# Performance work log

Measured on AMD Instinct MI355X. Metric: run time of the kernel, lower is better.

## Reference

```python
import jax, jax.numpy as jnp
import numpy as np

T, H, E, I, K = 2048, 2048, 16, 512, 2
ROUTED_SCALE = 1.5   # config.moe_router_scaling_factor
SWIGLU_LIMIT = 7.0   # config.swiglu_limits[layer_id]


def setup_inputs() -> dict:
    key = jax.random.key(0)
    k1, k2, k3, k4, k5 = jax.random.split(key, 5)
    hidden_states = jax.random.normal(k1, (T, H), jnp.float32)
    gate_w = jax.random.normal(k2, (E, H), jnp.float32) * 0.02
    router_bias = jax.random.normal(k3, (E,), jnp.float32) * 0.01
    w13 = jax.random.normal(k4, (E, 2 * I, H), jnp.float32) * 0.02  # [gate; up] fused
    w2 = jax.random.normal(k5, (E, H, I), jnp.float32) * 0.02
    return {"hidden_states": hidden_states, "gate_w": gate_w,
            "router_bias": router_bias, "w13": w13, "w2": w2, "top_k": K}


def reference(hidden_states, gate_w, router_bias, w13, w2, top_k):
    n_tok = hidden_states.shape[0]
    n_exp = gate_w.shape[0]
    # fp32 gate (need_fp32_gate=True)
    router_logits = hidden_states.astype(jnp.float32) @ gate_w.T          # [T, E]
    scores = jax.nn.sigmoid(router_logits)
    # correction bias only affects expert choice, not the combine weights
    _, topk_ids = jax.lax.top_k(scores + router_bias[None, :], top_k)     # [T, K]
    topk_w = jnp.take_along_axis(scores, topk_ids, axis=1)                # [T, K]
    topk_w = topk_w / jnp.sum(topk_w, axis=1, keepdims=True)              # renormalize
    topk_w = topk_w * ROUTED_SCALE
    # scatter routing weights into dense per-expert combine weights [T, E]
    comb = jnp.zeros((n_tok, n_exp), jnp.float32)
    comb = comb.at[jnp.arange(n_tok)[:, None], topk_ids].add(topk_w)
    # expert SwiGLU MLPs, dense over experts (zero combine weight == not routed)
    gu = jnp.einsum('th,eoh->teo', hidden_states, w13)                    # [T, E, 2I]
    g, u = jnp.split(gu, 2, axis=-1)
    g = jnp.minimum(g, SWIGLU_LIMIT)                                      # gemm1_clamp_limit
    u = jnp.clip(u, -SWIGLU_LIMIT, SWIGLU_LIMIT)
    act = g * jax.nn.sigmoid(g) * u                                       # silu(gate) * up
    expert_out = jnp.einsum('tei,ehi->teh', act, w2)                      # [T, E, H]
    return jnp.einsum('teh,te->th', expert_out, comb)                     # [T, H]
```

## Files before the change

### kernel.cpp

```cpp
#include <hip/hip_runtime.h>
#include <hip/hip_bf16.h>
#include <math.h>

#define T_TOK 2048
#define H_DIM 2048
#define E_EXP 16
#define I_DIM 512
#define TWO_I 1024
#define ROUTED_SCALE 1.5f
#define SWIGLU_LIMIT 7.0f

#define BM 64
#define KC 64
#define MAX_TILES 80

typedef __attribute__((ext_vector_type(8))) short bf16x8;
typedef __attribute__((ext_vector_type(4))) float f32x4;
typedef unsigned short u16;

__device__ inline u16 f2bf(float f) {
    return __builtin_bit_cast(u16, __float2bfloat16(f));
}
__device__ inline ushort4 pack4(float4 a) {
    ushort4 v;
    v.x = f2bf(a.x); v.y = f2bf(a.y); v.z = f2bf(a.z); v.w = f2bf(a.w);
    return v;
}

__device__ inline void gload16(const u16* g, u16* l) {
    __builtin_amdgcn_global_load_lds(
        (const __attribute__((address_space(1))) void*)(g),
        (__attribute__((address_space(3))) void*)(l), 16, 0, 0);
}

#define SWZ(row, k) ((row) * 64 + ((k) ^ (((row) & 7) << 3)))

__global__ __launch_bounds__(256) void router_kernel(
    const float* __restrict__ hs, const float* __restrict__ gw,
    const float* __restrict__ bias, int* cnt, int* tok_list, float* w_list,
    u16* __restrict__ hs_bf)
{
    int wave = threadIdx.x >> 6;
    int lane = threadIdx.x & 63;
    int t = blockIdx.x * 4 + wave;
    if (t >= T_TOK) return;
    const float* x = hs + (size_t)t * H_DIM;

    float acc[E_EXP];
#pragma unroll
    for (int e = 0; e < E_EXP; ++e) acc[e] = 0.f;

#pragma unroll 2
    for (int c = 0; c < 8; ++c) {
        int col = c * 256 + lane * 4;
        float4 xv = *(const float4*)(x + col);
        *(ushort4*)(hs_bf + (size_t)t * H_DIM + col) = pack4(xv);
#pragma unroll
        for (int e = 0; e < E_EXP; ++e) {
            float4 gv = *(const float4*)(gw + (size_t)e * H_DIM + col);
            acc[e] = fmaf(xv.x, gv.x, acc[e]);
            acc[e] = fmaf(xv.y, gv.y, acc[e]);
            acc[e] = fmaf(xv.z, gv.z, acc[e]);
            acc[e] = fmaf(xv.w, gv.w, acc[e]);
        }
    }
#pragma unroll
    for (int e = 0; e < E_EXP; ++e) {
        for (int m = 32; m >= 1; m >>= 1)
            acc[e] += __shfl_xor(acc[e], m, 64);
    }
    if (lane == 0) {
        float sc[E_EXP], bsc[E_EXP];
#pragma unroll
        for (int e = 0; e < E_EXP; ++e) {
            sc[e] = 1.f / (1.f + expf(-acc[e]));
            bsc[e] = sc[e] + bias[e];
        }
        int e0 = 0; float b0 = bsc[0];
#pragma unroll
        for (int e = 1; e < E_EXP; ++e) if (bsc[e] > b0) { b0 = bsc[e]; e0 = e; }
        int e1 = -1; float b1 = -1e30f;
#pragma unroll
        for (int e = 0; e < E_EXP; ++e) {
            if (e == e0) continue;
            if (bsc[e] > b1) { b1 = bsc[e]; e1 = e; }
        }
        float s0 = sc[e0], s1 = sc[e1];
        float inv = ROUTED_SCALE / (s0 + s1);
        int p0 = atomicAdd(&cnt[e0], 1);
        tok_list[e0 * T_TOK + p0] = t;
        w_list[e0 * T_TOK + p0] = s0 * inv;
        int p1 = atomicAdd(&cnt[e1], 1);
        tok_list[e1 * T_TOK + p1] = t;
        w_list[e1 * T_TOK + p1] = s1 * inv;
    }
}

__global__ void scatter_build(const int* __restrict__ cnt,
    const int* __restrict__ tok_list, const float* __restrict__ w_list,
    int* A_tok, float* A_w, int* tile_e, int* tile_r0)
{
    int c[E_EXP], offs[E_EXP + 1];
    offs[0] = 0;
#pragma unroll
    for (int e = 0; e < E_EXP; ++e) {
        c[e] = cnt[e];
        offs[e + 1] = offs[e] + ((c[e] + BM - 1) & ~(BM - 1));
    }
    int idx = blockIdx.x * 256 + threadIdx.x;
    int e = idx >> 11;
    int pos = idx & (T_TOK - 1);
    int ce = c[e];
    int pe = (ce + BM - 1) & ~(BM - 1);
    if (pos < ce) {
        A_tok[offs[e] + pos] = tok_list[idx];
        A_w[offs[e] + pos] = w_list[idx];
    } else if (pos < pe) {
        A_tok[offs[e] + pos] = -1;
        A_w[offs[e] + pos] = 0.f;
    }
    if (idx == 0) {
        int nt = 0;
        for (int ee = 0; ee < E_EXP; ++ee) {
            int ntile = (c[ee] + BM - 1) >> 6;
            for (int j = 0; j < ntile; ++j) {
                tile_e[nt] = ee;
                tile_r0[nt] = offs[ee] + j * BM;
                ++nt;
            }
        }
        for (; nt < MAX_TILES; ++nt) tile_e[nt] = -1;
    }
}

__global__ __launch_bounds__(256, 3) void gemm1_act(
    const u16* __restrict__ hs_bf, const float* __restrict__ w13,
    const int* __restrict__ A_tok, const int* __restrict__ tile_e,
    const int* __restrict__ tile_r0, u16* __restrict__ act)
{
    int b = blockIdx.x;
    int id = (b & 7) * 80 + (b >> 3);
    int tile = id % MAX_TILES;
    int y = id / MAX_TILES;
    int e = tile_e[tile];
    if (e < 0) return;
    int row0 = tile_r0[tile];
    int i0 = y * 64;
    int tid = threadIdx.x;

    __shared__ u16 Xs[2][4096];
    __shared__ u16 Gs[2][4096];
    __shared__ u16 Us[2][4096];

    const int l = tid & 63, w = tid >> 6;

    const int rlo = l >> 3;
    const int c8 = (l & 7) << 3;
    const int ksrc = c8 ^ (rlo << 3);
    const int rowA = w * 16 + rlo;
    const int rowB = rowA + 8;
    int tokA = A_tok[row0 + rowA]; if (tokA < 0) tokA = 0;
    int tokB = A_tok[row0 + rowB]; if (tokB < 0) tokB = 0;
    const u16* sXA = hs_bf + (size_t)tokA * H_DIM + ksrc;
    const u16* sXB = hs_bf + (size_t)tokB * H_DIM + ksrc;
    const int dA = w * 1024;

#define X_STAGE(bb, t) do { int ko = (t) * KC; \
    gload16(sXA + ko, &Xs[bb][dA]);  gload16(sXB + ko, &Xs[bb][dA + 512]); } while (0)

    const int srow = tid >> 4;
    const int sc4  = tid & 15;
    const int kphys = (sc4 * 4) ^ ((srow & 7) << 3);
    const int sbase = srow * 64 + kphys;
    const float* gsrc = w13 + ((size_t)e * TWO_I + i0 + srow) * H_DIM + sc4 * 4;
    const float* usrc = gsrc + (size_t)I_DIM * H_DIM;

    float4 gld[4], uld[4];
#define W_LOAD(t) do { int k0 = (t) * KC; \
    gld[0] = *(const float4*)(gsrc + k0); \
    gld[1] = *(const float4*)(gsrc + k0 + 16 * H_DIM); \
    gld[2] = *(const float4*)(gsrc + k0 + 32 * H_DIM); \
    gld[3] = *(const float4*)(gsrc + k0 + 48 * H_DIM); \
    uld[0] = *(const float4*)(usrc + k0); \
    uld[1] = *(const float4*)(usrc + k0 + 16 * H_DIM); \
    uld[2] = *(const float4*)(usrc + k0 + 32 * H_DIM); \
    uld[3] = *(const float4*)(usrc + k0 + 48 * H_DIM); } while (0)

#define W_WRITE(bb) do { \
    *(ushort4*)&Gs[bb][sbase]        = pack4(gld[0]); \
    *(ushort4*)&Gs[bb][sbase + 1024] = pack4(gld[1]); \
    *(ushort4*)&Gs[bb][sbase + 2048] = pack4(gld[2]); \
    *(ushort4*)&Gs[bb][sbase + 3072] = pack4(gld[3]); \
    *(ushort4*)&Us[bb][sbase]        = pack4(uld[0]); \
    *(ushort4*)&Us[bb][sbase + 1024] = pack4(uld[1]); \
    *(ushort4*)&Us[bb][sbase + 2048] = pack4(uld[2]); \
    *(ushort4*)&Us[bb][sbase + 3072] = pack4(uld[3]); } while (0)

    const int wm = w >> 1, wn = w & 1;
    const int lr = l & 15;
    const int lg = l >> 4;
    const int ra0 = wm * 32 + lr, ra1 = ra0 + 16;
    const int rb0 = wn * 32 + lr, rb1 = rb0 + 16;
    int ia0[2], ia1[2], ib0[2], ib1[2];
#pragma unroll
    for (int kh = 0; kh < 2; ++kh) {
        int e2 = kh * 32 + lg * 8;
        ia0[kh] = SWZ(ra0, e2); ia1[kh] = SWZ(ra1, e2);
        ib0[kh] = SWZ(rb0, e2); ib1[kh] = SWZ(rb1, e2);
    }

    const f32x4 Z4 = {0.f, 0.f, 0.f, 0.f};
    f32x4 aG[2][2], aU[2][2];
#pragma unroll
    for (int m = 0; m < 2; ++m)
#pragma unroll
        for (int n = 0; n < 2; ++n) { aG[m][n] = Z4; aU[m][n] = Z4; }

    W_LOAD(0);
    X_STAGE(0, 0);
    W_WRITE(0);
    __syncthreads();
    int cur = 0;
    const int NT = H_DIM / KC;
    for (int t = 0; t < NT; ++t) {
        const bool more = (t + 1 < NT);
        if (more) {
            X_STAGE(cur ^ 1, t + 1);
            W_LOAD(t + 1);
            __builtin_amdgcn_sched_barrier(0);
        }
#pragma unroll
        for (int kh = 0; kh < 2; ++kh) {
            bf16x8 a0 = *(const bf16x8*)&Xs[cur][ia0[kh]];
            bf16x8 a1 = *(const bf16x8*)&Xs[cur][ia1[kh]];
            bf16x8 g0 = *(const bf16x8*)&Gs[cur][ib0[kh]];
            bf16x8 g1 = *(const bf16x8*)&Gs[cur][ib1[kh]];
            bf16x8 u0 = *(const bf16x8*)&Us[cur][ib0[kh]];
            bf16x8 u1 = *(const bf16x8*)&Us[cur][ib1[kh]];
            aG[0][0] = __builtin_amdgcn_mfma_f32_16x16x32_bf16(a0, g0, aG[0][0], 0, 0, 0);
            aG[0][1] = __builtin_amdgcn_mfma_f32_16x16x32_bf16(a0, g1, aG[0][1], 0, 0, 0);
            aG[1][0] = __builtin_amdgcn_mfma_f32_16x16x32_bf16(a1, g0, aG[1][0], 0, 0, 0);
            aG[1][1] = __builtin_amdgcn_mfma_f32_16x16x32_bf16(a1, g1, aG[1][1], 0, 0, 0);
            aU[0][0] = __builtin_amdgcn_mfma_f32_16x16x32_bf16(a0, u0, aU[0][0], 0, 0, 0);
            aU[0][1] = __builtin_amdgcn_mfma_f32_16x16x32_bf16(a0, u1, aU[0][1], 0, 0, 0);
            aU[1][0] = __builtin_amdgcn_mfma_f32_16x16x32_bf16(a1, u0, aU[1][0], 0, 0, 0);
            aU[1][1] = __builtin_amdgcn_mfma_f32_16x16x32_bf16(a1, u1, aU[1][1], 0, 0, 0);
        }
        if (more) W_WRITE(cur ^ 1);
        __syncthreads();
        cur ^= 1;
    }
#undef X_STAGE
#undef W_LOAD
#undef W_WRITE

#pragma unroll
    for (int m = 0; m < 2; ++m)
#pragma unroll
        for (int n = 0; n < 2; ++n) {
            int col = i0 + wn * 32 + n * 16 + lr;
            int rbase = row0 + wm * 32 + m * 16 + lg * 4;
#pragma unroll
            for (int q = 0; q < 4; ++q) {
                float g = fminf(aG[m][n][q], SWIGLU_LIMIT);
                float u = fminf(fmaxf(aU[m][n][q], -SWIGLU_LIMIT), SWIGLU_LIMIT);
                float s = 1.f / (1.f + __expf(-g));
                act[(size_t)(rbase + q) * I_DIM + col] = f2bf(g * s * u);
            }
        }
}

__global__ __launch_bounds__(256, 3) void gemm2_scatter(
    const u16* __restrict__ act, const float* __restrict__ w2,
    const int* __restrict__ A_tok, const float* __restrict__ A_w,
    const int* __restrict__ tile_e, const int* __restrict__ tile_r0,
    float* __restrict__ out)
{
    int b = blockIdx.x;
    int id = (b & 7) * 320 + (b >> 3);
    int tile = id % MAX_TILES;
    int y = id / MAX_TILES;
    int e = tile_e[tile];
    if (e < 0) return;
    int row0 = tile_r0[tile];
    int h0 = y * 64;
    int tid = threadIdx.x;

    __shared__ u16 As[2][4096];
    __shared__ u16 Bs[2][4096];
    __shared__ int toks[BM];
    __shared__ float wts[BM];
    if (tid < BM) { toks[tid] = A_tok[row0 + tid]; wts[tid] = A_w[row0 + tid]; }

    const int l = tid & 63, w = tid >> 6;

    const int rlo = l >> 3;
    const int c8 = (l & 7) << 3;
    const int ksrc = c8 ^ (rlo << 3);
    const int rowA = w * 16 + rlo;
    const int rowB = rowA + 8;
    const u16* sAA = act + (size_t)(row0 + rowA) * I_DIM + ksrc;
    const u16* sAB = act + (size_t)(row0 + rowB) * I_DIM + ksrc;
    const int dA = w * 1024;

#define A_STAGE(bb, t) do { int ko = (t) * KC; \
    gload16(sAA + ko, &As[bb][dA]);  gload16(sAB + ko, &As[bb][dA + 512]); } while (0)

    const int srow = tid >> 4;
    const int sc4  = tid & 15;
    const int kphys = (sc4 * 4) ^ ((srow & 7) << 3);
    const int sbase = srow * 64 + kphys;
    const float* bsrc = w2 + ((size_t)e * H_DIM + h0 + srow) * I_DIM + sc4 * 4;

    float4 bld[4];
#define B_LOAD(t) do { int k0 = (t) * KC; \
    bld[0] = *(const float4*)(bsrc + k0); \
    bld[1] = *(const float4*)(bsrc + k0 + 16 * I_DIM); \
    bld[2] = *(const float4*)(bsrc + k0 + 32 * I_DIM); \
    bld[3] = *(const float4*)(bsrc + k0 + 48 * I_DIM); } while (0)

#define B_WRITE(bb) do { \
    *(ushort4*)&Bs[bb][sbase]        = pack4(bld[0]); \
    *(ushort4*)&Bs[bb][sbase + 1024] = pack4(bld[1]); \
    *(ushort4*)&Bs[bb][sbase + 2048] = pack4(bld[2]); \
    *(ushort4*)&Bs[bb][sbase + 3072] = pack4(bld[3]); } while (0)

    const int wm = w >> 1, wn = w & 1;
    const int lr = l & 15;
    const int lg = l >> 4;
    const int ra0 = wm * 32 + lr, ra1 = ra0 + 16;
    const int rb0 = wn * 32 + lr, rb1 = rb0 + 16;
    int ia0[2], ia1[2], ib0[2], ib1[2];
#pragma unroll
    for (int kh = 0; kh < 2; ++kh) {
        int e2 = kh * 32 + lg * 8;
        ia0[kh] = SWZ(ra0, e2); ia1[kh] = SWZ(ra1, e2);
        ib0[kh] = SWZ(rb0, e2); ib1[kh] = SWZ(rb1, e2);
    }

    const f32x4 Z4 = {0.f, 0.f, 0.f, 0.f};
    f32x4 acc[2][2];
#pragma unroll
    for (int m = 0; m < 2; ++m)
#pragma unroll
        for (int n = 0; n < 2; ++n) acc[m][n] = Z4;

    B_LOAD(0);
    A_STAGE(0, 0);
    B_WRITE(0);
    __syncthreads();
    int cur = 0;
    const int NT = I_DIM / KC;
    for (int t = 0; t < NT; ++t) {
        const bool more = (t + 1 < NT);
        if (more) {
            A_STAGE(cur ^ 1, t + 1);
            B_LOAD(t + 1);
            __builtin_amdgcn_sched_barrier(0);
        }
#pragma unroll
        for (int kh = 0; kh < 2; ++kh) {
            bf16x8 a0 = *(const bf16x8*)&As[cur][ia0[kh]];
            bf16x8 a1 = *(const bf16x8*)&As[cur][ia1[kh]];
            bf16x8 b0 = *(const bf16x8*)&Bs[cur][ib0[kh]];
            bf16x8 b1 = *(const bf16x8*)&Bs[cur][ib1[kh]];
            acc[0][0] = __builtin_amdgcn_mfma_f32_16x16x32_bf16(a0, b0, acc[0][0], 0, 0, 0);
            acc[0][1] = __builtin_amdgcn_mfma_f32_16x16x32_bf16(a0, b1, acc[0][1], 0, 0, 0);
            acc[1][0] = __builtin_amdgcn_mfma_f32_16x16x32_bf16(a1, b0, acc[1][0], 0, 0, 0);
            acc[1][1] = __builtin_amdgcn_mfma_f32_16x16x32_bf16(a1, b1, acc[1][1], 0, 0, 0);
        }
        if (more) B_WRITE(cur ^ 1);
        __syncthreads();
        cur ^= 1;
    }
#undef A_STAGE
#undef B_LOAD
#undef B_WRITE

#pragma unroll
    for (int m = 0; m < 2; ++m)
#pragma unroll
        for (int n = 0; n < 2; ++n) {
            int col = h0 + wn * 32 + n * 16 + lr;
            int sbase2 = wm * 32 + m * 16 + lg * 4;
#pragma unroll
            for (int q = 0; q < 4; ++q) {
                int slot = sbase2 + q;
                int tok = toks[slot];
                if (tok >= 0)
                    atomicAdd(&out[(size_t)tok * H_DIM + col], acc[m][n][q] * wts[slot]);
            }
        }
}

extern "C" void kernel_launch(void* const* d_in, const int* in_sizes, int n_in,
                              void* d_out, int out_size, void* d_ws, size_t ws_size,
                              hipStream_t stream) {
    const float* hs   = (const float*)d_in[0];
    const float* gw   = (const float*)d_in[1];
    const float* bias = (const float*)d_in[2];
    const float* w13  = (const float*)d_in[3];
    const float* w2   = (const float*)d_in[4];
    float* out = (float*)d_out;

    char* ws = (char*)d_ws;
    int*   cnt      = (int*)(ws + 0);
    int*   tile_e   = (int*)(ws + 64);
    int*   tile_r0  = (int*)(ws + 384);
    int*   tok_list = (int*)(ws + 1024);
    float* w_list   = (float*)(ws + 132096);
    int*   A_tok    = (int*)(ws + 263168);
    float* A_w      = (float*)(ws + 283648);
    u16*   act      = (u16*)(ws + 304128);
    u16*   hs_bf    = (u16*)(ws + 5547008);

    hipMemsetAsync(d_out, 0, (size_t)T_TOK * H_DIM * sizeof(float), stream);
    hipMemsetAsync(cnt, 0, 64, stream);

    router_kernel<<<T_TOK / 4, 256, 0, stream>>>(hs, gw, bias, cnt, tok_list, w_list, hs_bf);
    scatter_build<<<(E_EXP * T_TOK) / 256, 256, 0, stream>>>(cnt, tok_list, w_list, A_tok, A_w, tile_e, tile_r0);

    gemm1_act<<<MAX_TILES * 8, 256, 0, stream>>>(hs_bf, w13, A_tok, tile_e, tile_r0, act);
    gemm2_scatter<<<MAX_TILES * 32, 256, 0, stream>>>(act, w2, A_tok, A_w, tile_e, tile_r0, out);
}
```

Baseline: 178.0 us.

## Enlarge MoE GEMM row tiles to 128 tokens and widen weight staging loads

Doubles the per-expert token tile from 64 to 128 rows in both expert GEMMs, so each block computes 4x2 MFMA sub-tiles per wave. Each converted fp32 weight tile is therefore reused across twice as many tokens, which halves weight global reads and fp32-to-bf16 conversions per output. Weight staging switches to each thread loading 16 contiguous floats and writing 8-element bf16 vectors to LDS. The costs are more padding waste per expert, fewer blocks (48 tiles max), and higher LDS and register use, with occupancy hint lowered from 3 to 2.

```diff
diff --git a/kernel.cpp b/kernel.cpp
--- a/kernel.cpp
+++ b/kernel.cpp
@@ -10,9 +10,10 @@
 #define ROUTED_SCALE 1.5f
 #define SWIGLU_LIMIT 7.0f
 
-#define BM 64
+#define BM 128
 #define KC 64
-#define MAX_TILES 80
+#define MAX_TILES 48
+#define PADMAX 6144
 
 typedef __attribute__((ext_vector_type(8))) short bf16x8;
 typedef __attribute__((ext_vector_type(4))) float f32x4;
@@ -20,6 +21,14 @@
 
 __device__ inline u16 f2bf(float f) {
     return __builtin_bit_cast(u16, __float2bfloat16(f));
+}
+__device__ inline bf16x8 pack8(float4 a, float4 b) {
+    bf16x8 v;
+    v[0] = (short)f2bf(a.x); v[1] = (short)f2bf(a.y);
+    v[2] = (short)f2bf(a.z); v[3] = (short)f2bf(a.w);
+    v[4] = (short)f2bf(b.x); v[5] = (short)f2bf(b.y);
+    v[6] = (short)f2bf(b.z); v[7] = (short)f2bf(b.w);
+    return v;
 }
 __device__ inline ushort4 pack4(float4 a) {
     ushort4 v;
@@ -122,7 +131,7 @@
     if (idx == 0) {
         int nt = 0;
         for (int ee = 0; ee < E_EXP; ++ee) {
-            int ntile = (c[ee] + BM - 1) >> 6;
+            int ntile = (c[ee] + BM - 1) >> 7;
             for (int j = 0; j < ntile; ++j) {
                 tile_e[nt] = ee;
                 tile_r0[nt] = offs[ee] + j * BM;
@@ -133,13 +142,13 @@
     }
 }
 
-__global__ __launch_bounds__(256, 3) void gemm1_act(
+__global__ __launch_bounds__(256, 2) void gemm1_act(
     const u16* __restrict__ hs_bf, const float* __restrict__ w13,
     const int* __restrict__ A_tok, const int* __restrict__ tile_e,
     const int* __restrict__ tile_r0, u16* __restrict__ act)
 {
     int b = blockIdx.x;
-    int id = (b & 7) * 80 + (b >> 3);
+    int id = (b & 7) * MAX_TILES + (b >> 3);
     int tile = id % MAX_TILES;
     int y = id / MAX_TILES;
     int e = tile_e[tile];
@@ -148,7 +157,7 @@
     int i0 = y * 64;
     int tid = threadIdx.x;
 
-    __shared__ u16 Xs[2][4096];
+    __shared__ u16 Xs[2][8192];
     __shared__ u16 Gs[2][4096];
     __shared__ u16 Us[2][4096];
 
@@ -157,62 +166,57 @@
     const int rlo = l >> 3;
     const int c8 = (l & 7) << 3;
     const int ksrc = c8 ^ (rlo << 3);
-    const int rowA = w * 16 + rlo;
-    const int rowB = rowA + 8;
-    int tokA = A_tok[row0 + rowA]; if (tokA < 0) tokA = 0;
-    int tokB = A_tok[row0 + rowB]; if (tokB < 0) tokB = 0;
-    const u16* sXA = hs_bf + (size_t)tokA * H_DIM + ksrc;
-    const u16* sXB = hs_bf + (size_t)tokB * H_DIM + ksrc;
-    const int dA = w * 1024;
+    const u16* sX[4];
+#pragma unroll
+    for (int j = 0; j < 4; ++j) {
+        int row = w * 32 + j * 8 + rlo;
+        int tk = A_tok[row0 + row]; if (tk < 0) tk = 0;
+        sX[j] = hs_bf + (size_t)tk * H_DIM + ksrc;
+    }
+    const int dX = w * 2048;
 
 #define X_STAGE(bb, t) do { int ko = (t) * KC; \
-    gload16(sXA + ko, &Xs[bb][dA]);  gload16(sXB + ko, &Xs[bb][dA + 512]); } while (0)
-
-    const int srow = tid >> 4;
-    const int sc4  = tid & 15;
-    const int kphys = (sc4 * 4) ^ ((srow & 7) << 3);
-    const int sbase = srow * 64 + kphys;
-    const float* gsrc = w13 + ((size_t)e * TWO_I + i0 + srow) * H_DIM + sc4 * 4;
+    gload16(sX[0] + ko, &Xs[bb][dX]); \
+    gload16(sX[1] + ko, &Xs[bb][dX + 512]); \
+    gload16(sX[2] + ko, &Xs[bb][dX + 1024]); \
+    gload16(sX[3] + ko, &Xs[bb][dX + 1536]); } while (0)
+
+    const int srow = tid >> 2;
+    const int c2 = tid & 3;
+    const float* gsrc = w13 + ((size_t)e * TWO_I + i0 + srow) * H_DIM + c2 * 16;
     const float* usrc = gsrc + (size_t)I_DIM * H_DIM;
-
-    float4 gld[4], uld[4];
+    const int wbA = SWZ(srow, c2 * 16);
+    const int wbB = SWZ(srow, c2 * 16 + 8);
+
+    float4 ga0, ga1, gb0, gb1, ua0, ua1, ub0, ub1;
 #define W_LOAD(t) do { int k0 = (t) * KC; \
-    gld[0] = *(const float4*)(gsrc + k0); \
-    gld[1] = *(const float4*)(gsrc + k0 + 16 * H_DIM); \
-    gld[2] = *(const float4*)(gsrc + k0 + 32 * H_DIM); \
-    gld[3] = *(const float4*)(gsrc + k0 + 48 * H_DIM); \
-    uld[0] = *(const float4*)(usrc + k0); \
-    uld[1] = *(const float4*)(usrc + k0 + 16 * H_DIM); \
-    uld[2] = *(const float4*)(usrc + k0 + 32 * H_DIM); \
-    uld[3] = *(const float4*)(usrc + k0 + 48 * H_DIM); } while (0)
+    ga0 = *(const float4*)(gsrc + k0);      ga1 = *(const float4*)(gsrc + k0 + 4); \
+    gb0 = *(const float4*)(gsrc + k0 + 8);  gb1 = *(const float4*)(gsrc + k0 + 12); \
+    ua0 = *(const float4*)(usrc + k0);      ua1 = *(const float4*)(usrc + k0 + 4); \
+    ub0 = *(const float4*)(usrc + k0 + 8);  ub1 = *(const float4*)(usrc + k0 + 12); } while (0)
 
 #define W_WRITE(bb) do { \
-    *(ushort4*)&Gs[bb][sbase]        = pack4(gld[0]); \
-    *(ushort4*)&Gs[bb][sbase + 1024] = pack4(gld[1]); \
-    *(ushort4*)&Gs[bb][sbase + 2048] = pack4(gld[2]); \
-    *(ushort4*)&Gs[bb][sbase + 3072] = pack4(gld[3]); \
-    *(ushort4*)&Us[bb][sbase]        = pack4(uld[0]); \
-    *(ushort4*)&Us[bb][sbase + 1024] = pack4(uld[1]); \
-    *(ushort4*)&Us[bb][sbase + 2048] = pack4(uld[2]); \
-    *(ushort4*)&Us[bb][sbase + 3072] = pack4(uld[3]); } while (0)
+    *(bf16x8*)&Gs[bb][wbA] = pack8(ga0, ga1); \
+    *(bf16x8*)&Gs[bb][wbB] = pack8(gb0, gb1); \
+    *(bf16x8*)&Us[bb][wbA] = pack8(ua0, ua1); \
+    *(bf16x8*)&Us[bb][wbB] = pack8(ub0, ub1); } while (0)
 
     const int wm = w >> 1, wn = w & 1;
-    const int lr = l & 15;
-    const int lg = l >> 4;
-    const int ra0 = wm * 32 + lr, ra1 = ra0 + 16;
-    const int rb0 = wn * 32 + lr, rb1 = rb0 + 16;
-    int ia0[2], ia1[2], ib0[2], ib1[2];
+    const int lr = l & 15, lg = l >> 4;
+    int ia[4][2], ib[2][2];
 #pragma unroll
     for (int kh = 0; kh < 2; ++kh) {
         int e2 = kh * 32 + lg * 8;
-        ia0[kh] = SWZ(ra0, e2); ia1[kh] = SWZ(ra1, e2);
-        ib0[kh] = SWZ(rb0, e2); ib1[kh] = SWZ(rb1, e2);
+#pragma unroll
+        for (int m = 0; m < 4; ++m) ia[m][kh] = SWZ(wm * 64 + m * 16 + lr, e2);
+#pragma unroll
+        for (int n = 0; n < 2; ++n) ib[n][kh] = SWZ(wn * 32 + n * 16 + lr, e2);
     }
 
     const f32x4 Z4 = {0.f, 0.f, 0.f, 0.f};
-    f32x4 aG[2][2], aU[2][2];
-#pragma unroll
-    for (int m = 0; m < 2; ++m)
+    f32x4 aG[4][2], aU[4][2];
+#pragma unroll
+    for (int m = 0; m < 4; ++m)
 #pragma unroll
         for (int n = 0; n < 2; ++n) { aG[m][n] = Z4; aU[m][n] = Z4; }
 
@@ -231,20 +235,30 @@
         }
 #pragma unroll
         for (int kh = 0; kh < 2; ++kh) {
-            bf16x8 a0 = *(const bf16x8*)&Xs[cur][ia0[kh]];
-            bf16x8 a1 = *(const bf16x8*)&Xs[cur][ia1[kh]];
-            bf16x8 g0 = *(const bf16x8*)&Gs[cur][ib0[kh]];
-            bf16x8 g1 = *(const bf16x8*)&Gs[cur][ib1[kh]];
-            bf16x8 u0 = *(const bf16x8*)&Us[cur][ib0[kh]];
-            bf16x8 u1 = *(const bf16x8*)&Us[cur][ib1[kh]];
+            bf16x8 a0 = *(const bf16x8*)&Xs[cur][ia[0][kh]];
+            bf16x8 a1 = *(const bf16x8*)&Xs[cur][ia[1][kh]];
+            bf16x8 a2 = *(const bf16x8*)&Xs[cur][ia[2][kh]];
+            bf16x8 a3 = *(const bf16x8*)&Xs[cur][ia[3][kh]];
+            bf16x8 g0 = *(const bf16x8*)&Gs[cur][ib[0][kh]];
+            bf16x8 g1 = *(const bf16x8*)&Gs[cur][ib[1][kh]];
+            bf16x8 u0 = *(const bf16x8*)&Us[cur][ib[0][kh]];
+            bf16x8 u1 = *(const bf16x8*)&Us[cur][ib[1][kh]];
             aG[0][0] = __builtin_amdgcn_mfma_f32_16x16x32_bf16(a0, g0, aG[0][0], 0, 0, 0);
             aG[0][1] = __builtin_amdgcn_mfma_f32_16x16x32_bf16(a0, g1, aG[0][1], 0, 0, 0);
             aG[1][0] = __builtin_amdgcn_mfma_f32_16x16x32_bf16(a1, g0, aG[1][0], 0, 0, 0);
             aG[1][1] = __builtin_amdgcn_mfma_f32_16x16x32_bf16(a1, g1, aG[1][1], 0, 0, 0);
+            aG[2][0] = __builtin_amdgcn_mfma_f32_16x16x32_bf16(a2, g0, aG[2][0], 0, 0, 0);
+            aG[2][1] = __builtin_amdgcn_mfma_f32_16x16x32_bf16(a2, g1, aG[2][1], 0, 0, 0);
+            aG[3][0] = __builtin_amdgcn_mfma_f32_16x16x32_bf16(a3, g0, aG[3][0], 0, 0, 0);
+            aG[3][1] = __builtin_amdgcn_mfma_f32_16x16x32_bf16(a3, g1, aG[3][1], 0, 0, 0);
             aU[0][0] = __builtin_amdgcn_mfma_f32_16x16x32_bf16(a0, u0, aU[0][0], 0, 0, 0);
             aU[0][1] = __builtin_amdgcn_mfma_f32_16x16x32_bf16(a0, u1, aU[0][1], 0, 0, 0);
             aU[1][0] = __builtin_amdgcn_mfma_f32_16x16x32_bf16(a1, u0, aU[1][0], 0, 0, 0);
             aU[1][1] = __builtin_amdgcn_mfma_f32_16x16x32_bf16(a1, u1, aU[1][1], 0, 0, 0);
+            aU[2][0] = __builtin_amdgcn_mfma_f32_16x16x32_bf16(a2, u0, aU[2][0], 0, 0, 0);
+            aU[2][1] = __builtin_amdgcn_mfma_f32_16x16x32_bf16(a2, u1, aU[2][1], 0, 0, 0);
+            aU[3][0] = __builtin_amdgcn_mfma_f32_16x16x32_bf16(a3, u0, aU[3][0], 0, 0, 0);
+            aU[3][1] = __builtin_amdgcn_mfma_f32_16x16x32_bf16(a3, u1, aU[3][1], 0, 0, 0);
         }
         if (more) W_WRITE(cur ^ 1);
         __syncthreads();
@@ -255,11 +269,11 @@
 #undef W_WRITE
 
 #pragma unroll
-    for (int m = 0; m < 2; ++m)
+    for (int m = 0; m < 4; ++m)
 #pragma unroll
         for (int n = 0; n < 2; ++n) {
             int col = i0 + wn * 32 + n * 16 + lr;
-            int rbase = row0 + wm * 32 + m * 16 + lg * 4;
+            int rbase = row0 + wm * 64 + m * 16 + lg * 4;
 #pragma unroll
             for (int q = 0; q < 4; ++q) {
                 float g = fminf(aG[m][n][q], SWIGLU_LIMIT);
@@ -277,7 +291,7 @@
     float* __restrict__ out)
 {
     int b = blockIdx.x;
-    int id = (b & 7) * 320 + (b >> 3);
+    int id = (b & 7) * 192 + (b >> 3);
     int tile = id % MAX_TILES;
     int y = id / MAX_TILES;
     int e = tile_e[tile];
@@ -286,7 +300,7 @@
     int h0 = y * 64;
     int tid = threadIdx.x;
 
-    __shared__ u16 As[2][4096];
+    __shared__ u16 As[2][8192];
     __shared__ u16 Bs[2][4096];
     __shared__ int toks[BM];
     __shared__ float wts[BM];
@@ -297,51 +311,51 @@
     const int rlo = l >> 3;
     const int c8 = (l & 7) << 3;
     const int ksrc = c8 ^ (rlo << 3);
-    const int rowA = w * 16 + rlo;
-    const int rowB = rowA + 8;
-    const u16* sAA = act + (size_t)(row0 + rowA) * I_DIM + ksrc;
-    const u16* sAB = act + (size_t)(row0 + rowB) * I_DIM + ksrc;
-    const int dA = w * 1024;
+    const u16* sA[4];
+#pragma unroll
+    for (int j = 0; j < 4; ++j) {
+        int row = w * 32 + j * 8 + rlo;
+        sA[j] = act + (size_t)(row0 + row) * I_DIM + ksrc;
+    }
+    const int dA = w * 2048;
 
 #define A_STAGE(bb, t) do { int ko = (t) * KC; \
-    gload16(sAA + ko, &As[bb][dA]);  gload16(sAB + ko, &As[bb][dA + 512]); } while (0)
-
-    const int srow = tid >> 4;
-    const int sc4  = tid & 15;
-    const int kphys = (sc4 * 4) ^ ((srow & 7) << 3);
-    const int sbase = srow * 64 + kphys;
-    const float* bsrc = w2 + ((size_t)e * H_DIM + h0 + srow) * I_DIM + sc4 * 4;
-
-    float4 bld[4];
+    gload16(sA[0] + ko, &As[bb][dA]); \
+    gload16(sA[1] + ko, &As[bb][dA + 512]); \
+    gload16(sA[2] + ko, &As[bb][dA + 1024]); \
+    gload16(sA[3] + ko, &As[bb][dA + 1536]); } while (0)
+
+    const int srow = tid >> 2;
+    const int c2 = tid & 3;
+    const float* bsrc = w2 + ((size_t)e * H_DIM + h0 + srow) * I_DIM + c2 * 16;
+    const int wbA = SWZ(srow, c2 * 16);
+    const int wbB = SWZ(srow, c2 * 16 + 8);
+
+    float4 ba0, ba1, bb0, bb1;
 #define B_LOAD(t) do { int k0 = (t) * KC; \
-    bld[0] = *(const float4*)(bsrc + k0); \
-    bld[1] = *(const float4*)(bsrc + k0 + 16 * I_DIM); \
-    bld[2] = *(const float4*)(bsrc + k0 + 32 * I_DIM); \
-    bld[3] = *(const float4*)(bsrc + k0 + 48 * I_DIM); } while (0)
+    ba0 = *(const float4*)(bsrc + k0);      ba1 = *(const float4*)(bsrc + k0 + 4); \
+    bb0 = *(const float4*)(bsrc + k0 + 8);  bb1 = *(const float4*)(bsrc + k0 + 12); } while (0)
 
 #define B_WRITE(bb) do { \
-    *(ushort4*)&Bs[bb][sbase]        = pack4(bld[0]); \
-    *(ushort4*)&Bs[bb][sbase + 1024] = pack4(bld[1]); \
-    *(ushort4*)&Bs[bb][sbase + 2048] = pack4(bld[2]); \
-    *(ushort4*)&Bs[bb][sbase + 3072] = pack4(bld[3]); } while (0)
+    *(bf16x8*)&Bs[bb][wbA] = pack8(ba0, ba1); \
+    *(bf16x8*)&Bs[bb][wbB] = pack8(bb0, bb1); } while (0)
 
     const int wm = w >> 1, wn = w & 1;
-    const int lr = l & 15;
-    const int lg = l >> 4;
-    const int ra0 = wm * 32 + lr, ra1 = ra0 + 16;
-    const int rb0 = wn * 32 + lr, rb1 = rb0 + 16;
-    int ia0[2], ia1[2], ib0[2], ib1[2];
+    const int lr = l & 15, lg = l >> 4;
+    int ia[4][2], ib[2][2];
 #pragma unroll
     for (int kh = 0; kh < 2; ++kh) {
         int e2 = kh * 32 + lg * 8;
-        ia0[kh] = SWZ(ra0, e2); ia1[kh] = SWZ(ra1, e2);
-        ib0[kh] = SWZ(rb0, e2); ib1[kh] = SWZ(rb1, e2);
+#pragma unroll
+        for (int m = 0; m < 4; ++m) ia[m][kh] = SWZ(wm * 64 + m * 16 + lr, e2);
+#pragma unroll
+        for (int n = 0; n < 2; ++n) ib[n][kh] = SWZ(wn * 32 + n * 16 + lr, e2);
     }
 
     const f32x4 Z4 = {0.f, 0.f, 0.f, 0.f};
-    f32x4 acc[2][2];
-#pragma unroll
-    for (int m = 0; m < 2; ++m)
+    f32x4 acc[4][2];
+#pragma unroll
+    for (int m = 0; m < 4; ++m)
 #pragma unroll
         for (int n = 0; n < 2; ++n) acc[m][n] = Z4;
 
@@ -360,14 +374,20 @@
         }
 #pragma unroll
         for (int kh = 0; kh < 2; ++kh) {
-            bf16x8 a0 = *(const bf16x8*)&As[cur][ia0[kh]];
-            bf16x8 a1 = *(const bf16x8*)&As[cur][ia1[kh]];
-            bf16x8 b0 = *(const bf16x8*)&Bs[cur][ib0[kh]];
-            bf16x8 b1 = *(const bf16x8*)&Bs[cur][ib1[kh]];
+            bf16x8 a0 = *(const bf16x8*)&As[cur][ia[0][kh]];
+            bf16x8 a1 = *(const bf16x8*)&As[cur][ia[1][kh]];
+            bf16x8 a2 = *(const bf16x8*)&As[cur][ia[2][kh]];
+            bf16x8 a3 = *(const bf16x8*)&As[cur][ia[3][kh]];
+            bf16x8 b0 = *(const bf16x8*)&Bs[cur][ib[0][kh]];
+            bf16x8 b1 = *(const bf16x8*)&Bs[cur][ib[1][kh]];
             acc[0][0] = __builtin_amdgcn_mfma_f32_16x16x32_bf16(a0, b0, acc[0][0], 0, 0, 0);
             acc[0][1] = __builtin_amdgcn_mfma_f32_16x16x32_bf16(a0, b1, acc[0][1], 0, 0, 0);
             acc[1][0] = __builtin_amdgcn_mfma_f32_16x16x32_bf16(a1, b0, acc[1][0], 0, 0, 0);
             acc[1][1] = __builtin_amdgcn_mfma_f32_16x16x32_bf16(a1, b1, acc[1][1], 0, 0, 0);
+            acc[2][0] = __builtin_amdgcn_mfma_f32_16x16x32_bf16(a2, b0, acc[2][0], 0, 0, 0);
+            acc[2][1] = __builtin_amdgcn_mfma_f32_16x16x32_bf16(a2, b1, acc[2][1], 0, 0, 0);
+            acc[3][0] = __builtin_amdgcn_mfma_f32_16x16x32_bf16(a3, b0, acc[3][0], 0, 0, 0);
+            acc[3][1] = __builtin_amdgcn_mfma_f32_16x16x32_bf16(a3, b1, acc[3][1], 0, 0, 0);
         }
         if (more) B_WRITE(cur ^ 1);
         __syncthreads();
@@ -378,14 +398,14 @@
 #undef B_WRITE
 
 #pragma unroll
-    for (int m = 0; m < 2; ++m)
+    for (int m = 0; m < 4; ++m)
 #pragma unroll
         for (int n = 0; n < 2; ++n) {
             int col = h0 + wn * 32 + n * 16 + lr;
-            int sbase2 = wm * 32 + m * 16 + lg * 4;
+            int sbase = wm * 64 + m * 16 + lg * 4;
 #pragma unroll
             for (int q = 0; q < 4; ++q) {
-                int slot = sbase2 + q;
+                int slot = sbase + q;
                 int tok = toks[slot];
                 if (tok >= 0)
                     atomicAdd(&out[(size_t)tok * H_DIM + col], acc[m][n][q] * wts[slot]);
@@ -406,13 +426,13 @@
     char* ws = (char*)d_ws;
     int*   cnt      = (int*)(ws + 0);
     int*   tile_e   = (int*)(ws + 64);
-    int*   tile_r0  = (int*)(ws + 384);
+    int*   tile_r0  = (int*)(ws + 320);
     int*   tok_list = (int*)(ws + 1024);
     float* w_list   = (float*)(ws + 132096);
     int*   A_tok    = (int*)(ws + 263168);
-    float* A_w      = (float*)(ws + 283648);
-    u16*   act      = (u16*)(ws + 304128);
-    u16*   hs_bf    = (u16*)(ws + 5547008);
+    float* A_w      = (float*)(ws + 287744);
+    u16*   act      = (u16*)(ws + 315392);
+    u16*   hs_bf    = (u16*)(ws + 6606848);
 
     hipMemsetAsync(d_out, 0, (size_t)T_TOK * H_DIM * sizeof(float), stream);
     hipMemsetAsync(cnt, 0, 64, stream);
```

Result: no change. 178.9 us (+0.5%).

## Widen gemm2 output tile to 128 columns with 32-wide K chunks

Applied to the files above, without the earlier changes.

Reworks the second expert GEMM so each block computes a 64x128 output tile with a K chunk of 32 instead of 64x64 with K chunk 64. Each wave now issues eight MFMAs per stage against four B fragments, the grid is halved, and the occupancy hint rises to 4 blocks per CU. The token and weight lookups move from shared memory to direct global reads in the epilogue. The aim is more reuse of each act tile per block and fewer blocks re-reading act. The cost is twice as many K iterations, each with its own barrier, and more accumulator registers, which may not fit the higher occupancy target.

```diff
diff --git a/kernel.cpp b/kernel.cpp
--- a/kernel.cpp
+++ b/kernel.cpp
@@ -12,6 +12,7 @@
 
 #define BM 64
 #define KC 64
+#define KC2 32
 #define MAX_TILES 80
 
 typedef __attribute__((ext_vector_type(8))) short bf16x8;
@@ -26,12 +27,21 @@
     v.x = f2bf(a.x); v.y = f2bf(a.y); v.z = f2bf(a.z); v.w = f2bf(a.w);
     return v;
 }
+__device__ inline bf16x8 pack8(float4 a, float4 b) {
+    bf16x8 v;
+    v[0] = (short)f2bf(a.x); v[1] = (short)f2bf(a.y);
+    v[2] = (short)f2bf(a.z); v[3] = (short)f2bf(a.w);
+    v[4] = (short)f2bf(b.x); v[5] = (short)f2bf(b.y);
+    v[6] = (short)f2bf(b.z); v[7] = (short)f2bf(b.w);
+    return v;
+}
 
 __device__ inline void gload16(const u16* g, u16* l) {
     __builtin_amdgcn_global_load_lds(
         (const __attribute__((address_space(1))) void*)(g),
         (__attribute__((address_space(3))) void*)(l), 16, 0, 0);
 }
+#define SCHED0() __builtin_amdgcn_sched_barrier(0)
 
 #define SWZ(row, k) ((row) * 64 + ((k) ^ (((row) & 7) << 3)))
 
@@ -227,7 +237,7 @@
         if (more) {
             X_STAGE(cur ^ 1, t + 1);
             W_LOAD(t + 1);
-            __builtin_amdgcn_sched_barrier(0);
+            SCHED0();
         }
 #pragma unroll
         for (int kh = 0; kh < 2; ++kh) {
@@ -270,104 +280,97 @@
         }
 }
 
-__global__ __launch_bounds__(256, 3) void gemm2_scatter(
+__global__ __launch_bounds__(256, 4) void gemm2_scatter(
     const u16* __restrict__ act, const float* __restrict__ w2,
     const int* __restrict__ A_tok, const float* __restrict__ A_w,
     const int* __restrict__ tile_e, const int* __restrict__ tile_r0,
     float* __restrict__ out)
 {
     int b = blockIdx.x;
-    int id = (b & 7) * 320 + (b >> 3);
+    int id = (b & 7) * 160 + (b >> 3);
     int tile = id % MAX_TILES;
     int y = id / MAX_TILES;
     int e = tile_e[tile];
     if (e < 0) return;
     int row0 = tile_r0[tile];
-    int h0 = y * 64;
+    int h0 = y * 128;
     int tid = threadIdx.x;
 
-    __shared__ u16 As[2][4096];
+    __shared__ u16 As[2][2048];
     __shared__ u16 Bs[2][4096];
-    __shared__ int toks[BM];
-    __shared__ float wts[BM];
-    if (tid < BM) { toks[tid] = A_tok[row0 + tid]; wts[tid] = A_w[row0 + tid]; }
 
     const int l = tid & 63, w = tid >> 6;
 
-    const int rlo = l >> 3;
-    const int c8 = (l & 7) << 3;
-    const int ksrc = c8 ^ (rlo << 3);
-    const int rowA = w * 16 + rlo;
-    const int rowB = rowA + 8;
-    const u16* sAA = act + (size_t)(row0 + rowA) * I_DIM + ksrc;
-    const u16* sAB = act + (size_t)(row0 + rowB) * I_DIM + ksrc;
-    const int dA = w * 1024;
-
-#define A_STAGE(bb, t) do { int ko = (t) * KC; \
-    gload16(sAA + ko, &As[bb][dA]);  gload16(sAB + ko, &As[bb][dA + 512]); } while (0)
-
-    const int srow = tid >> 4;
-    const int sc4  = tid & 15;
-    const int kphys = (sc4 * 4) ^ ((srow & 7) << 3);
-    const int sbase = srow * 64 + kphys;
-    const float* bsrc = w2 + ((size_t)e * H_DIM + h0 + srow) * I_DIM + sc4 * 4;
-
-    float4 bld[4];
-#define B_LOAD(t) do { int k0 = (t) * KC; \
-    bld[0] = *(const float4*)(bsrc + k0); \
-    bld[1] = *(const float4*)(bsrc + k0 + 16 * I_DIM); \
-    bld[2] = *(const float4*)(bsrc + k0 + 32 * I_DIM); \
-    bld[3] = *(const float4*)(bsrc + k0 + 48 * I_DIM); } while (0)
-
+    {
+    }
+    const int arow = w * 16 + (l >> 2);
+    const int sg = (l & 3) ^ ((l >> 3) & 3);
+    const u16* sA = act + (size_t)(row0 + arow) * I_DIM + sg * 8;
+    const int dA = w * 512;
+
+#define A_STAGE(bb, t) do { int ko = (t) * KC2; \
+    gload16(sA + ko, &As[bb][dA]); } while (0)
+
+    const int wr = tid >> 1;
+    const int g0 = (tid & 1) * 2;
+    const int g1 = g0 + 1;
+    const float* bsrc = w2 + ((size_t)e * H_DIM + h0 + wr) * I_DIM + g0 * 8;
+    const int wswz = (wr >> 1) & 3;
+    const int wd0 = wr * 32 + (g0 ^ wswz) * 8;
+    const int wd1 = wr * 32 + (g1 ^ wswz) * 8;
+
+    float4 b0a, b0b, b1a, b1b;
+#define B_LOAD(t) do { int ko = (t) * KC2; \
+    b0a = *(const float4*)(bsrc + ko);      b0b = *(const float4*)(bsrc + ko + 4); \
+    b1a = *(const float4*)(bsrc + ko + 8);  b1b = *(const float4*)(bsrc + ko + 12); } while (0)
 #define B_WRITE(bb) do { \
-    *(ushort4*)&Bs[bb][sbase]        = pack4(bld[0]); \
-    *(ushort4*)&Bs[bb][sbase + 1024] = pack4(bld[1]); \
-    *(ushort4*)&Bs[bb][sbase + 2048] = pack4(bld[2]); \
-    *(ushort4*)&Bs[bb][sbase + 3072] = pack4(bld[3]); } while (0)
+    *(bf16x8*)&Bs[bb][wd0] = pack8(b0a, b0b); \
+    *(bf16x8*)&Bs[bb][wd1] = pack8(b1a, b1b); } while (0)
 
     const int wm = w >> 1, wn = w & 1;
-    const int lr = l & 15;
-    const int lg = l >> 4;
-    const int ra0 = wm * 32 + lr, ra1 = ra0 + 16;
-    const int rb0 = wn * 32 + lr, rb1 = rb0 + 16;
-    int ia0[2], ia1[2], ib0[2], ib1[2];
-#pragma unroll
-    for (int kh = 0; kh < 2; ++kh) {
-        int e2 = kh * 32 + lg * 8;
-        ia0[kh] = SWZ(ra0, e2); ia1[kh] = SWZ(ra1, e2);
-        ib0[kh] = SWZ(rb0, e2); ib1[kh] = SWZ(rb1, e2);
-    }
+    const int lr = l & 15, lg = l >> 4;
+    const int swz = (lg ^ ((lr >> 1) & 3)) * 8;
+    int ix[2], ib[4];
+#pragma unroll
+    for (int m = 0; m < 2; ++m) ix[m] = (wm * 32 + m * 16 + lr) * 32 + swz;
+#pragma unroll
+    for (int n = 0; n < 4; ++n) ib[n] = (wn * 64 + n * 16 + lr) * 32 + swz;
 
     const f32x4 Z4 = {0.f, 0.f, 0.f, 0.f};
-    f32x4 acc[2][2];
+    f32x4 acc[2][4];
 #pragma unroll
     for (int m = 0; m < 2; ++m)
 #pragma unroll
-        for (int n = 0; n < 2; ++n) acc[m][n] = Z4;
+        for (int n = 0; n < 4; ++n) acc[m][n] = Z4;
 
     B_LOAD(0);
     A_STAGE(0, 0);
     B_WRITE(0);
     __syncthreads();
     int cur = 0;
-    const int NT = I_DIM / KC;
+    const int NT = I_DIM / KC2;
     for (int t = 0; t < NT; ++t) {
         const bool more = (t + 1 < NT);
         if (more) {
             A_STAGE(cur ^ 1, t + 1);
             B_LOAD(t + 1);
-            __builtin_amdgcn_sched_barrier(0);
-        }
-#pragma unroll
-        for (int kh = 0; kh < 2; ++kh) {
-            bf16x8 a0 = *(const bf16x8*)&As[cur][ia0[kh]];
-            bf16x8 a1 = *(const bf16x8*)&As[cur][ia1[kh]];
-            bf16x8 b0 = *(const bf16x8*)&Bs[cur][ib0[kh]];
-            bf16x8 b1 = *(const bf16x8*)&Bs[cur][ib1[kh]];
-            acc[0][0] = __builtin_amdgcn_mfma_f32_16x16x32_bf16(a0, b0, acc[0][0], 0, 0, 0);
-            acc[0][1] = __builtin_amdgcn_mfma_f32_16x16x32_bf16(a0, b1, acc[0][1], 0, 0, 0);
-            acc[1][0] = __builtin_amdgcn_mfma_f32_16x16x32_bf16(a1, b0, acc[1][0], 0, 0, 0);
-            acc[1][1] = __builtin_amdgcn_mfma_f32_16x16x32_bf16(a1, b1, acc[1][1], 0, 0, 0);
+            SCHED0();
+        }
+        {
+            bf16x8 a0 = *(const bf16x8*)&As[cur][ix[0]];
+            bf16x8 a1 = *(const bf16x8*)&As[cur][ix[1]];
+            bf16x8 v0 = *(const bf16x8*)&Bs[cur][ib[0]];
+            bf16x8 v1 = *(const bf16x8*)&Bs[cur][ib[1]];
+            bf16x8 v2 = *(const bf16x8*)&Bs[cur][ib[2]];
+            bf16x8 v3 = *(const bf16x8*)&Bs[cur][ib[3]];
+            acc[0][0] = __builtin_amdgcn_mfma_f32_16x16x32_bf16(a0, v0, acc[0][0], 0, 0, 0);
+            acc[0][1] = __builtin_amdgcn_mfma_f32_16x16x32_bf16(a0, v1, acc[0][1], 0, 0, 0);
+            acc[0][2] = __builtin_amdgcn_mfma_f32_16x16x32_bf16(a0, v2, acc[0][2], 0, 0, 0);
+            acc[0][3] = __builtin_amdgcn_mfma_f32_16x16x32_bf16(a0, v3, acc[0][3], 0, 0, 0);
+            acc[1][0] = __builtin_amdgcn_mfma_f32_16x16x32_bf16(a1, v0, acc[1][0], 0, 0, 0);
+            acc[1][1] = __builtin_amdgcn_mfma_f32_16x16x32_bf16(a1, v1, acc[1][1], 0, 0, 0);
+            acc[1][2] = __builtin_amdgcn_mfma_f32_16x16x32_bf16(a1, v2, acc[1][2], 0, 0, 0);
+            acc[1][3] = __builtin_amdgcn_mfma_f32_16x16x32_bf16(a1, v3, acc[1][3], 0, 0, 0);
         }
         if (more) B_WRITE(cur ^ 1);
         __syncthreads();
@@ -380,15 +383,15 @@
 #pragma unroll
     for (int m = 0; m < 2; ++m)
 #pragma unroll
-        for (int n = 0; n < 2; ++n) {
-            int col = h0 + wn * 32 + n * 16 + lr;
-            int sbase2 = wm * 32 + m * 16 + lg * 4;
+        for (int n = 0; n < 4; ++n) {
+            int col = h0 + wn * 64 + n * 16 + lr;
+            int sbase = wm * 32 + m * 16 + lg * 4;
 #pragma unroll
             for (int q = 0; q < 4; ++q) {
-                int slot = sbase2 + q;
-                int tok = toks[slot];
+                int slot = row0 + sbase + q;
+                int tok = A_tok[slot];
                 if (tok >= 0)
-                    atomicAdd(&out[(size_t)tok * H_DIM + col], acc[m][n][q] * wts[slot]);
+                    atomicAdd(&out[(size_t)tok * H_DIM + col], acc[m][n][q] * A_w[slot]);
             }
         }
 }
@@ -421,5 +424,5 @@
     scatter_build<<<(E_EXP * T_TOK) / 256, 256, 0, stream>>>(cnt, tok_list, w_list, A_tok, A_w, tile_e, tile_r0);
 
     gemm1_act<<<MAX_TILES * 8, 256, 0, stream>>>(hs_bf, w13, A_tok, tile_e, tile_r0, act);
-    gemm2_scatter<<<MAX_TILES * 32, 256, 0, stream>>>(act, w2, A_tok, A_w, tile_e, tile_r0, out);
-}
+    gemm2_scatter<<<MAX_TILES * 16, 256, 0, stream>>>(act, w2, A_tok, A_w, tile_e, tile_r0, out);
+}
```

Result: slower. 185.4 us (+4.1%).
